# Kernel optimization log

Hardware: AMD Instinct MI355X
Metric: run time of the kernel (lower is better)

Reference implementation:

```python
import jax, jax.numpy as jnp
import numpy as np

NBITS = 4
OUT_F = 2048
IN_F = 2048


def _bit_ste(w, nbits):
    # clamp to [-1,1], quantize magnitude to nbits levels, keep sign
    step = float(2 ** nbits - 1)
    w = jnp.clip(w, -1.0, 1.0)
    return jnp.round(jnp.abs(w) * step) / step * jnp.sign(w)


def setup_inputs() -> dict:
    key = jax.random.key(0)
    ks = jax.random.split(key, 6)
    ex = np.arange(NBITS - 1, -1, -1)
    exps = jnp.asarray(2.0 ** ex / (2.0 ** NBITS - 1), dtype=jnp.float32)
    inp = {
        "input": jax.random.normal(ks[0], (8, 2048, IN_F), dtype=jnp.float32),
        # bit-plane weights: sigmoid of these gives soft bits in (0,1)
        "pweight": jax.random.normal(ks[1], (OUT_F, IN_F, NBITS), dtype=jnp.float32),
        "nweight": jax.random.normal(ks[2], (OUT_F, IN_F, NBITS), dtype=jnp.float32),
        "exps": exps,
        "bexps": exps,
        "mask_weight": jnp.ones((NBITS,), dtype=jnp.float32),  # init.constant_(1)
        "scale": jnp.array([0.05], dtype=jnp.float32),
        "pbias": jax.random.uniform(ks[3], (OUT_F, NBITS), dtype=jnp.float32, minval=0.0, maxval=float(2 ** NBITS - 1)) // 1.0 % 2.0,
        "nbias": jax.random.uniform(ks[4], (OUT_F, NBITS), dtype=jnp.float32, minval=0.0, maxval=float(2 ** NBITS - 1)) // 1.0 % 2.0,
        "biasscale": jnp.array([0.05], dtype=jnp.float32),
    }
    return inp


def reference(input, pweight, nweight, exps, bexps, mask_weight, scale, pbias, nbias, biasscale):
    temp = 1.0
    # temp_s and mask_discrete are all-ones buffers -> identity factors
    mask = jax.nn.sigmoid(mask_weight)                      # [N]
    soft = jax.nn.sigmoid(temp * pweight) - jax.nn.sigmoid(temp * nweight)  # [O,I,N]
    weight = jnp.einsum('oin,n->oi', soft, exps * mask) * scale[0]          # [O,I]
    bias_raw = jnp.einsum('on,n->o', pbias - nbias, bexps)  # [O]
    bias = _bit_ste(bias_raw, NBITS) * biasscale[0]
    # F.linear: y = x @ W^T + b
    return jnp.einsum('bsi,oi->bso', input, weight) + bias
```

## Files before the change

### kernel.cpp

```cpp
#include <hip/hip_runtime.h>
#include <hip/hip_bf16.h>
#include <stdint.h>

#define M_DIM 16384
#define N_DIM 2048
#define K_DIM 2048

typedef __attribute__((ext_vector_type(8))) __bf16 bf16x8;
typedef __attribute__((ext_vector_type(4))) float f32x4;

__device__ __forceinline__ unsigned short f2bf(float f) {
  unsigned int u = __builtin_bit_cast(unsigned int, f);
  u += 0x7FFFu + ((u >> 16) & 1u);
  return (unsigned short)(u >> 16);
}

__device__ __forceinline__ float sigmoidf_(float x) {
  return 1.0f / (1.0f + __expf(-x));
}

__global__ __launch_bounds__(256) void convert_x(const float4* __restrict__ x,
                                                 uint4* __restrict__ xb) {
  int idx = blockIdx.x * 256 + threadIdx.x;
  float4 a = x[idx * 2];
  float4 b = x[idx * 2 + 1];
  uint4 r;
  r.x = (unsigned)f2bf(a.x) | ((unsigned)f2bf(a.y) << 16);
  r.y = (unsigned)f2bf(a.z) | ((unsigned)f2bf(a.w) << 16);
  r.z = (unsigned)f2bf(b.x) | ((unsigned)f2bf(b.y) << 16);
  r.w = (unsigned)f2bf(b.z) | ((unsigned)f2bf(b.w) << 16);
  xb[idx] = r;
}

__global__ __launch_bounds__(256) void make_w(const float4* __restrict__ pw,
                                              const float4* __restrict__ nw,
                                              const float* __restrict__ exps,
                                              const float* __restrict__ maskw,
                                              const float* __restrict__ scale,
                                              unsigned short* __restrict__ wout) {
  const int beta = blockIdx.x;
  const int xcd = beta & 7;
  const int j = beta >> 3;
  const int o = xcd * 256 + (j >> 3);
  const int iblk = j & 7;
  int idx = (o * 2048 + iblk * 256) + threadIdx.x;
  float4 p = pw[idx];
  float4 n = nw[idx];
  float s = scale[0];
  float c0 = sigmoidf_(maskw[0]) * exps[0] * s;
  float c1 = sigmoidf_(maskw[1]) * exps[1] * s;
  float c2 = sigmoidf_(maskw[2]) * exps[2] * s;
  float c3 = sigmoidf_(maskw[3]) * exps[3] * s;
  float w = (sigmoidf_(p.x) - sigmoidf_(n.x)) * c0
          + (sigmoidf_(p.y) - sigmoidf_(n.y)) * c1
          + (sigmoidf_(p.z) - sigmoidf_(n.z)) * c2
          + (sigmoidf_(p.w) - sigmoidf_(n.w)) * c3;
  wout[idx] = f2bf(w);
}

__global__ __launch_bounds__(256) void make_bias(const float* __restrict__ pb,
                                                 const float* __restrict__ nb,
                                                 const float* __restrict__ bexps,
                                                 const float* __restrict__ bscale,
                                                 float* __restrict__ bias) {
  int o = blockIdx.x * 256 + threadIdx.x;
  if (o < N_DIM) {
    float x = 0.f;
#pragma unroll
    for (int n = 0; n < 4; ++n) x += (pb[o * 4 + n] - nb[o * 4 + n]) * bexps[n];
    float xc = fminf(fmaxf(x, -1.f), 1.f);
    float mag = rintf(fabsf(xc) * 15.f) * (1.f / 15.f);
    float sgn = (xc > 0.f) ? 1.f : ((xc < 0.f) ? -1.f : 0.f);
    bias[o] = mag * sgn * bscale[0];
  }
}


#define BM 256
#define BN 256
#define BK 64
#define NT (K_DIM / BK)

__device__ __forceinline__ void gload16(const void* g, void* l) {
  __builtin_amdgcn_global_load_lds(
      (const __attribute__((address_space(1))) unsigned int*)g,
      (__attribute__((address_space(3))) unsigned int*)l, 16, 0, 0);
}

#define VMCNT(n) asm volatile("s_waitcnt vmcnt(" #n ")" ::: "memory")
#define BAR() __builtin_amdgcn_s_barrier()

__global__ __launch_bounds__(512, 2) void gemm_bias(const unsigned short* __restrict__ X,
                                                    const unsigned short* __restrict__ W,
                                                    const float* __restrict__ bias,
                                                    float* __restrict__ out) {
  __shared__ unsigned short sA[2][BM * BK];
  __shared__ unsigned short sB[2][BN * BK];

  const int tid = threadIdx.x;
  const int bn = (int)blockIdx.x & 7;
  const int bm = (int)blockIdx.x >> 3;
  const int row0 = bm * BM, col0 = bn * BN;

  const int w = tid >> 6, l = tid & 63;
  const int wr = w >> 2;
  const int wc = w & 3;
  const int lr = l & 15;
  const int lk4 = l >> 4;
  const int l7 = l & 7;

  const unsigned short* Ag = X + (size_t)row0 * K_DIM;
  const unsigned short* Bg = W + (size_t)col0 * K_DIM;

  const int srl = (tid >> 3) & 31;
  const int sc16 = (tid & 7) ^ ((tid >> 3) & 7);
  const int shi = tid >> 8;
  const int slin = ((tid >> 3) & 24) * 64 + (tid & 63) * 8;

  auto stage = [&](unsigned short* lbase, const unsigned short* gbase,
                   int rb0, int rb1, int tk) {
    int rb = shi ? rb1 : rb0;
    int trow = rb + srl;
    gload16(gbase + (size_t)trow * K_DIM + tk * BK + sc16 * 8,
            lbase + rb * 64 + slin);
  };

  auto rdA = [&](const unsigned short* base, int mf, int ks) -> bf16x8 {
    int trow = wr * 128 + mf * 16 + lr;
    int c16l = (ks * 4 + lk4) ^ l7;
    return *(const bf16x8*)&base[trow * 64 + c16l * 8];
  };
  auto rdB = [&](const unsigned short* base, int nf, int ks) -> bf16x8 {
    int trow = wc * 64 + nf * 16 + lr;
    int c16l = (ks * 4 + lk4) ^ l7;
    return *(const bf16x8*)&base[trow * 64 + c16l * 8];
  };

  f32x4 acc[8][4] = {};
  bf16x8 a[4][2], b[4][2];

#define PHASE_MFMA(mh, nh)                                                    \
  __builtin_amdgcn_s_setprio(1);                                              \
  _Pragma("unroll") for (int i = 0; i < 4; ++i)                               \
  _Pragma("unroll") for (int j = 0; j < 2; ++j)                               \
  _Pragma("unroll") for (int ks = 0; ks < 2; ++ks)                            \
      acc[(mh) * 4 + i][(nh) * 2 + j] = __builtin_amdgcn_mfma_f32_16x16x32_bf16( \
          a[i][ks], b[(nh) * 2 + j][ks], acc[(mh) * 4 + i][(nh) * 2 + j], 0, 0, 0); \
  __builtin_amdgcn_s_setprio(0);

  {
    unsigned short* qa = sA[0];
    unsigned short* qb = sB[0];
    stage(qa, Ag, 0, 32, 0);
    stage(qa, Ag, 128, 160, 0);
    stage(qb, Bg, 0, 64, 0);
    stage(qb, Bg, 128, 192, 0);
    stage(qb, Bg, 32, 96, 0);
    stage(qb, Bg, 160, 224, 0);
    stage(qa, Ag, 64, 96, 0);
    stage(qa, Ag, 192, 224, 0);
  }
  VMCNT(4);
  BAR();

  for (int t = 0; t < NT; ++t) {
    const int p = t & 1, q = p ^ 1;
    const bool last = (t == NT - 1);
    const unsigned short* pa = sA[p];
    const unsigned short* pb = sB[p];
    unsigned short* qa = sA[q];
    unsigned short* qb = sB[q];

#pragma unroll
    for (int i = 0; i < 4; ++i)
#pragma unroll
      for (int ks = 0; ks < 2; ++ks) a[i][ks] = rdA(pa, i, ks);
#pragma unroll
    for (int j = 0; j < 2; ++j)
#pragma unroll
      for (int ks = 0; ks < 2; ++ks) b[j][ks] = rdB(pb, j, ks);
    if (!last) { stage(qa, Ag, 0, 32, t + 1); stage(qa, Ag, 128, 160, t + 1); }
    PHASE_MFMA(0, 0);
    if (!last) { VMCNT(4); } else { VMCNT(2); }
    BAR();

#pragma unroll
    for (int j = 2; j < 4; ++j)
#pragma unroll
      for (int ks = 0; ks < 2; ++ks) b[j][ks] = rdB(pb, j, ks);
    if (!last) { stage(qb, Bg, 0, 64, t + 1); stage(qb, Bg, 128, 192, t + 1); }
    PHASE_MFMA(0, 1);
    if (!last) { VMCNT(4); } else { VMCNT(0); }
    BAR();

#pragma unroll
    for (int i = 0; i < 4; ++i)
#pragma unroll
      for (int ks = 0; ks < 2; ++ks) a[i][ks] = rdA(pa, 4 + i, ks);
    if (!last) { stage(qb, Bg, 32, 96, t + 1); stage(qb, Bg, 160, 224, t + 1); }
    PHASE_MFMA(1, 0);
    BAR();

    if (!last) { stage(qa, Ag, 64, 96, t + 1); stage(qa, Ag, 192, 224, t + 1); }
    PHASE_MFMA(1, 1);
    if (!last) { VMCNT(4); }
    BAR();
  }

  float bv[4];
#pragma unroll
  for (int nf = 0; nf < 4; ++nf) bv[nf] = bias[col0 + wc * 64 + nf * 16 + lr];
  const int orow = lk4 * 4;
#pragma unroll
  for (int mf = 0; mf < 8; ++mf) {
#pragma unroll
    for (int nf = 0; nf < 4; ++nf) {
      const int colg = col0 + wc * 64 + nf * 16 + lr;
#pragma unroll
      for (int r = 0; r < 4; ++r) {
        int rowg = row0 + wr * 128 + mf * 16 + orow + r;
        out[(size_t)rowg * N_DIM + colg] = acc[mf][nf][r] + bv[nf];
      }
    }
  }
#undef PHASE_MFMA
}

extern "C" void kernel_launch(void* const* d_in, const int* in_sizes, int n_in,
                              void* d_out, int out_size, void* d_ws, size_t ws_size,
                              hipStream_t stream) {
  const float* input  = (const float*)d_in[0];
  const float* pweight = (const float*)d_in[1];
  const float* nweight = (const float*)d_in[2];
  const float* exps   = (const float*)d_in[3];
  const float* bexps  = (const float*)d_in[4];
  const float* maskw  = (const float*)d_in[5];
  const float* scale  = (const float*)d_in[6];
  const float* pbias  = (const float*)d_in[7];
  const float* nbias  = (const float*)d_in[8];
  const float* bscale = (const float*)d_in[9];
  float* out = (float*)d_out;

  unsigned short* Xb = (unsigned short*)d_ws;
  unsigned short* Wb = (unsigned short*)((char*)d_ws + (size_t)M_DIM * K_DIM * 2);
  float* bias = (float*)((char*)d_ws + (size_t)M_DIM * K_DIM * 2 + (size_t)N_DIM * K_DIM * 2);

  convert_x<<<(M_DIM * (size_t)K_DIM) / 8 / 256, 256, 0, stream>>>((const float4*)input, (uint4*)Xb);
  make_w<<<((size_t)N_DIM * K_DIM) / 256, 256, 0, stream>>>(
      (const float4*)pweight, (const float4*)nweight, exps, maskw, scale, Wb);
  make_bias<<<(N_DIM + 255) / 256, 256, 0, stream>>>(pbias, nbias, bexps, bscale, bias);

  dim3 grid((M_DIM / BM) * (N_DIM / BN));
  gemm_bias<<<grid, 512, 0, stream>>>(Xb, Wb, bias, out);
}
```

Measured before the change: 202.1 us.

## Switch GEMM to four-stage LDS pipeline with BK=32 and repacked tile layout

Replaces the double-buffered BK=64 pipeline, which had four barrier-separated phases per iteration, with a four-buffer ring using BK=32. Loads are issued three tiles ahead and there is one barrier per iteration. The LDS tile layout is repacked so that each 128x64 buffer holds two 128-row halves side by side in k, and the swizzled read addressing changes to match. The goal is to hide global-load latency better and cut barrier count, at the cost of more iterations, fewer MFMAs per sync, and wasted loads that wrap around in the final iterations.

```diff
diff --git a/kernel.cpp b/kernel.cpp
--- a/kernel.cpp
+++ b/kernel.cpp
@@ -78,8 +78,9 @@
 
 #define BM 256
 #define BN 256
-#define BK 64
+#define BK 32
 #define NT (K_DIM / BK)
+#define NBUF 4
 
 __device__ __forceinline__ void gload16(const void* g, void* l) {
   __builtin_amdgcn_global_load_lds(
@@ -94,8 +95,8 @@
                                                     const unsigned short* __restrict__ W,
                                                     const float* __restrict__ bias,
                                                     float* __restrict__ out) {
-  __shared__ unsigned short sA[2][BM * BK];
-  __shared__ unsigned short sB[2][BN * BK];
+  __shared__ unsigned short sA[NBUF][128 * 64];
+  __shared__ unsigned short sB[NBUF][128 * 64];
 
   const int tid = threadIdx.x;
   const int bn = (int)blockIdx.x & 7;
@@ -107,103 +108,73 @@
   const int wc = w & 3;
   const int lr = l & 15;
   const int lk4 = l >> 4;
-  const int l7 = l & 7;
+  const int lr7 = lr & 7;
 
   const unsigned short* Ag = X + (size_t)row0 * K_DIM;
   const unsigned short* Bg = W + (size_t)col0 * K_DIM;
 
-  const int srl = (tid >> 3) & 31;
-  const int sc16 = (tid & 7) ^ ((tid >> 3) & 7);
-  const int shi = tid >> 8;
-  const int slin = ((tid >> 3) & 24) * 64 + (tid & 63) * 8;
+  const int s_frl = tid >> 3;
+  const int s_pre = (tid & 7) ^ ((tid >> 3) & 7);
+  const int s_rglo = 128 * (s_pre >> 2);
+  const int s_k = (s_pre & 3) * 8;
+  const int s_dst = tid * 8;
 
   auto stage = [&](unsigned short* lbase, const unsigned short* gbase,
-                   int rb0, int rb1, int tk) {
-    int rb = shi ? rb1 : rb0;
-    int trow = rb + srl;
-    gload16(gbase + (size_t)trow * K_DIM + tk * BK + sc16 * 8,
-            lbase + rb * 64 + slin);
+                   int rr, int tk) {
+    gload16(gbase + (size_t)(rr + s_frl + s_rglo) * K_DIM + tk * BK + s_k,
+            lbase + rr * 64 + s_dst);
   };
 
-  auto rdA = [&](const unsigned short* base, int mf, int ks) -> bf16x8 {
-    int trow = wr * 128 + mf * 16 + lr;
-    int c16l = (ks * 4 + lk4) ^ l7;
-    return *(const bf16x8*)&base[trow * 64 + c16l * 8];
+  auto rdA = [&](const unsigned short* base, int mf) -> bf16x8 {
+    int fr = mf * 16 + lr;
+    int slot = (lk4 + 4 * wr) ^ lr7;
+    return *(const bf16x8*)&base[fr * 64 + slot * 8];
   };
-  auto rdB = [&](const unsigned short* base, int nf, int ks) -> bf16x8 {
-    int trow = wc * 64 + nf * 16 + lr;
-    int c16l = (ks * 4 + lk4) ^ l7;
-    return *(const bf16x8*)&base[trow * 64 + c16l * 8];
+  auto rdB = [&](const unsigned short* base, int nf) -> bf16x8 {
+    int fr = (wc & 1) * 64 + nf * 16 + lr;
+    int slot = (lk4 + 4 * (wc >> 1)) ^ lr7;
+    return *(const bf16x8*)&base[fr * 64 + slot * 8];
   };
 
   f32x4 acc[8][4] = {};
-  bf16x8 a[4][2], b[4][2];
-
-#define PHASE_MFMA(mh, nh)                                                    \
-  __builtin_amdgcn_s_setprio(1);                                              \
-  _Pragma("unroll") for (int i = 0; i < 4; ++i)                               \
-  _Pragma("unroll") for (int j = 0; j < 2; ++j)                               \
-  _Pragma("unroll") for (int ks = 0; ks < 2; ++ks)                            \
-      acc[(mh) * 4 + i][(nh) * 2 + j] = __builtin_amdgcn_mfma_f32_16x16x32_bf16( \
-          a[i][ks], b[(nh) * 2 + j][ks], acc[(mh) * 4 + i][(nh) * 2 + j], 0, 0, 0); \
-  __builtin_amdgcn_s_setprio(0);
-
-  {
-    unsigned short* qa = sA[0];
-    unsigned short* qb = sB[0];
-    stage(qa, Ag, 0, 32, 0);
-    stage(qa, Ag, 128, 160, 0);
-    stage(qb, Bg, 0, 64, 0);
-    stage(qb, Bg, 128, 192, 0);
-    stage(qb, Bg, 32, 96, 0);
-    stage(qb, Bg, 160, 224, 0);
-    stage(qa, Ag, 64, 96, 0);
-    stage(qa, Ag, 192, 224, 0);
-  }
-  VMCNT(4);
+  bf16x8 a[8], b[4];
+
+#pragma unroll
+  for (int pt = 0; pt < 3; ++pt) {
+    stage(sA[pt], Ag, 0, pt);
+    stage(sA[pt], Ag, 64, pt);
+    stage(sB[pt], Bg, 0, pt);
+    stage(sB[pt], Bg, 64, pt);
+  }
+  VMCNT(8);
   BAR();
 
   for (int t = 0; t < NT; ++t) {
-    const int p = t & 1, q = p ^ 1;
-    const bool last = (t == NT - 1);
-    const unsigned short* pa = sA[p];
-    const unsigned short* pb = sB[p];
-    unsigned short* qa = sA[q];
-    unsigned short* qb = sB[q];
-
-#pragma unroll
-    for (int i = 0; i < 4; ++i)
-#pragma unroll
-      for (int ks = 0; ks < 2; ++ks) a[i][ks] = rdA(pa, i, ks);
-#pragma unroll
-    for (int j = 0; j < 2; ++j)
-#pragma unroll
-      for (int ks = 0; ks < 2; ++ks) b[j][ks] = rdB(pb, j, ks);
-    if (!last) { stage(qa, Ag, 0, 32, t + 1); stage(qa, Ag, 128, 160, t + 1); }
-    PHASE_MFMA(0, 0);
-    if (!last) { VMCNT(4); } else { VMCNT(2); }
-    BAR();
-
-#pragma unroll
-    for (int j = 2; j < 4; ++j)
-#pragma unroll
-      for (int ks = 0; ks < 2; ++ks) b[j][ks] = rdB(pb, j, ks);
-    if (!last) { stage(qb, Bg, 0, 64, t + 1); stage(qb, Bg, 128, 192, t + 1); }
-    PHASE_MFMA(0, 1);
-    if (!last) { VMCNT(4); } else { VMCNT(0); }
-    BAR();
-
-#pragma unroll
-    for (int i = 0; i < 4; ++i)
-#pragma unroll
-      for (int ks = 0; ks < 2; ++ks) a[i][ks] = rdA(pa, 4 + i, ks);
-    if (!last) { stage(qb, Bg, 32, 96, t + 1); stage(qb, Bg, 160, 224, t + 1); }
-    PHASE_MFMA(1, 0);
-    BAR();
-
-    if (!last) { stage(qa, Ag, 64, 96, t + 1); stage(qa, Ag, 192, 224, t + 1); }
-    PHASE_MFMA(1, 1);
-    if (!last) { VMCNT(4); }
+    const unsigned short* pa = sA[t & 3];
+    const unsigned short* pb = sB[t & 3];
+    unsigned short* qa = sA[(t + 3) & 3];
+    unsigned short* qb = sB[(t + 3) & 3];
+    const int tk3 = (t + 3) & (NT - 1);
+#pragma unroll
+    for (int mf = 0; mf < 8; ++mf) a[mf] = rdA(pa, mf);
+#pragma unroll
+    for (int nf = 0; nf < 4; ++nf) b[nf] = rdB(pb, nf);
+
+    stage(qa, Ag, 0, tk3);
+    stage(qa, Ag, 64, tk3);
+    stage(qb, Bg, 0, tk3);
+    stage(qb, Bg, 64, tk3);
+
+    __builtin_amdgcn_s_setprio(1);
+#pragma unroll
+    for (int mf = 0; mf < 8; ++mf)
+#pragma unroll
+      for (int nf = 0; nf < 4; ++nf)
+        acc[mf][nf] = __builtin_amdgcn_mfma_f32_16x16x32_bf16(
+            a[mf], b[nf], acc[mf][nf], 0, 0, 0);
+    __builtin_amdgcn_s_setprio(0);
+
+    VMCNT(8);
     BAR();
   }
 
@@ -223,7 +194,6 @@
       }
     }
   }
-#undef PHASE_MFMA
 }
 
 extern "C" void kernel_launch(void* const* d_in, const int* in_sizes, int n_in,
```

Measured after the change: 201.7 us. No clear change (-0.2%).
